# Optimization experiments

Measured on AMD Instinct MI355X. Metric: run time of the kernel, lower is better.

## Reference

```python
import jax, jax.numpy as jnp
import numpy as np

N_EMBD = 768
FULL_SIZE = 16 * N_EMBD   # 12288
K = 4 * N_EMBD            # iter_size = 3072 (top-k)
B, T = 8, 1024


def setup_inputs() -> dict:
    key = jax.random.key(0)
    k0, k1, k2, k3, k4 = jax.random.split(key, 5)
    s = lambda fan_in: 1.0 / np.sqrt(fan_in)
    return {
        "x": jax.random.normal(k0, (B, T, N_EMBD), dtype=jnp.float32),
        "w1": jax.random.normal(k1, (N_EMBD // 16, N_EMBD), dtype=jnp.float32) * s(N_EMBD),
        "w2": jax.random.normal(k2, (FULL_SIZE, N_EMBD // 16), dtype=jnp.float32) * s(N_EMBD // 16),
        "w_mfc": jax.random.normal(k3, (FULL_SIZE, N_EMBD), dtype=jnp.float32) * s(N_EMBD),
        "w_proj": jax.random.normal(k4, (N_EMBD, FULL_SIZE), dtype=jnp.float32) * s(FULL_SIZE),
    }


def _topk_mask(ck, k):
    # softmax -> top-k indices -> hard 0/1 mask (scatter of constant 1.0)
    probs = jax.nn.softmax(ck, axis=-1)
    _, idx = jax.lax.top_k(probs, k)            # (B, k)
    b = jnp.arange(probs.shape[0])[:, None]
    return jnp.zeros_like(probs).at[b, idx].set(1.0)


def reference(x, w1, w2, w_mfc, w_proj):
    # control net on sequence-mean pooled features
    pooled = x.mean(axis=1)                                  # (B, D)
    ck = jax.nn.relu(pooled @ w1.T) @ w2.T                   # (B, F)
    mask = _topk_mask(ck, K)                                 # (B, F) hard 0/1
    # DynamicMaskedLinear: bmm(x, (W*mask)^T) == (x @ W^T) * mask (0/1 output mask)
    h = jnp.einsum('btd,fd->btf', x, w_mfc) * mask[:, None, :]
    h = jax.nn.relu(h)
    out = jnp.einsum('btf,ef->bte', h, w_proj)               # (B, T, D)
    return out
```

## Files before the change

kernel.cpp:

```cpp
#include <hip/hip_runtime.h>

#define N_EMBD 768
#define FULL   12288
#define KSEL   3072
#define BATCH  8
#define TLEN   1024
#define HID    48

typedef short bf16x8 __attribute__((ext_vector_type(8)));
typedef float f32x4 __attribute__((ext_vector_type(4)));
typedef unsigned short u16x4 __attribute__((ext_vector_type(4)));
typedef unsigned short u16x8 __attribute__((ext_vector_type(8)));

#define MFMA(a, b, c) __builtin_amdgcn_mfma_f32_16x16x32_bf16((a), (b), (c), 0, 0, 0)
#define GLDS(g, l) __builtin_amdgcn_global_load_lds( \
    (const __attribute__((address_space(1))) void*)(const void*)(g), \
    (__attribute__((address_space(3))) void*)(void*)(l), 16, 0, 0)

__device__ __forceinline__ unsigned short f2bf(float f) {
  unsigned u = __float_as_uint(f);
  u += 0x7fffu + ((u >> 16) & 1u);
  return (unsigned short)(u >> 16);
}
__device__ __forceinline__ float bf2f(unsigned short h) {
  return __uint_as_float(((unsigned)h) << 16);
}

__global__ void split_pool_x(const float* __restrict__ x, unsigned short* __restrict__ xh,
                             float* __restrict__ partial) {
  const int s = blockIdx.x;
  const int b = blockIdx.y;
  const int d = blockIdx.z * 256 + threadIdx.x * 4;
  const float* base = x + ((size_t)(b * TLEN + s * 64)) * N_EMBD + d;
  float4 sum = {0.f, 0.f, 0.f, 0.f};
  for (int t = 0; t < 64; ++t) {
    const float4 v = *(const float4*)(base + (size_t)t * N_EMBD);
    sum.x += v.x; sum.y += v.y; sum.z += v.z; sum.w += v.w;
    u16x4 h;
    h.x = f2bf(v.x); h.y = f2bf(v.y); h.z = f2bf(v.z); h.w = f2bf(v.w);
    *(u16x4*)(xh + ((size_t)(b * TLEN + s * 64 + t)) * N_EMBD + d) = h;
  }
  float* pp = partial + (b * 16 + s) * N_EMBD + d;
  pp[0] = sum.x; pp[1] = sum.y; pp[2] = sum.z; pp[3] = sum.w;
}

__global__ __launch_bounds__(256) void control1_kernel(
    const float* __restrict__ partial, const float* __restrict__ w1, float* __restrict__ hid) {
  __shared__ float w1s[HID][385];
  __shared__ float ps[N_EMBD];
  const int b = blockIdx.x;
  const int tid = threadIdx.x;
  for (int d = tid; d < N_EMBD; d += 256) {
    float sum = 0.f;
    #pragma unroll
    for (int s = 0; s < 16; ++s) sum += partial[(b * 16 + s) * N_EMBD + d];
    ps[d] = sum * (1.f / TLEN);
  }
  float acc = 0.f;
  #pragma unroll
  for (int half = 0; half < 2; ++half) {
    __syncthreads();
    for (int i = tid; i < HID * 384; i += 256) {
      const int r = i / 384, c = i % 384;
      w1s[r][c] = w1[r * N_EMBD + half * 384 + c];
    }
    __syncthreads();
    if (tid < HID) {
      const float* pr = ps + half * 384;
      #pragma unroll 8
      for (int d2 = 0; d2 < 384; ++d2) acc = fmaf(pr[d2], w1s[tid][d2], acc);
    }
  }
  if (tid < HID) hid[b * HID + tid] = fmaxf(acc, 0.f);
}

__global__ void control2_kernel(const float* __restrict__ hid, const float* __restrict__ w2,
                                float* __restrict__ ck) {
  const int b = blockIdx.y;
  const int f = blockIdx.x * 256 + threadIdx.x;
  __shared__ float hid_s[HID];
  if (threadIdx.x < HID) hid_s[threadIdx.x] = hid[b * HID + threadIdx.x];
  __syncthreads();
  const float* wr = w2 + (size_t)f * HID;
  float acc = 0.f;
  #pragma unroll
  for (int j = 0; j < HID; ++j) acc = fmaf(hid_s[j], wr[j], acc);
  ck[b * FULL + f] = acc;
}

__global__ void topk_kernel(const float* __restrict__ ck, int* __restrict__ sel) {
  const int b = blockIdx.x;
  const int tid = threadIdx.x;
  const int lane = tid & 63, wv = tid >> 6;
  unsigned key[48];
  const int f_lo = tid * 48;
  #pragma unroll
  for (int i = 0; i < 48; ++i) {
    unsigned u = __float_as_uint(ck[b * FULL + f_lo + i]);
    key[i] = (u & 0x80000000u) ? ~u : (u | 0x80000000u);
  }
  __shared__ unsigned redw[4];
  __shared__ int sg[257], se[257];
  unsigned prefix = 0;
  int remaining = KSEL;
  for (int bit = 31; bit >= 0; --bit) {
    const unsigned want = prefix | (1u << bit);
    const unsigned shifted = want >> bit;
    int cnt = 0;
    #pragma unroll
    for (int i = 0; i < 48; ++i) cnt += ((key[i] >> bit) == shifted) ? 1 : 0;
    #pragma unroll
    for (int off = 1; off < 64; off <<= 1) cnt += __shfl_xor(cnt, off, 64);
    if (lane == 0) redw[wv] = (unsigned)cnt;
    __syncthreads();
    const int c = (int)(redw[0] + redw[1] + redw[2] + redw[3]);
    __syncthreads();
    if (c >= remaining) prefix = want;
    else remaining -= c;
  }
  const unsigned kth = prefix;
  int cg = 0, ce = 0;
  #pragma unroll
  for (int i = 0; i < 48; ++i) { cg += (key[i] > kth) ? 1 : 0; ce += (key[i] == kth) ? 1 : 0; }
  sg[tid] = cg; se[tid] = ce;
  __syncthreads();
  if (tid == 0) {
    int ag = 0, ae = 0;
    for (int i = 0; i < 256; ++i) {
      int tg = sg[i], te = se[i];
      sg[i] = ag; se[i] = ae;
      ag += tg; ae += te;
    }
    sg[256] = ag;
  }
  __syncthreads();
  const int ng = sg[256];
  int gpos = sg[tid], epos = se[tid];
  #pragma unroll
  for (int i = 0; i < 48; ++i) {
    const unsigned k = key[i];
    const int f = f_lo + i;
    if (k > kth) {
      sel[b * KSEL + (gpos++)] = f;
    } else if (k == kth) {
      const int p = ng + epos;
      if (p < KSEL) sel[b * KSEL + p] = f;
      ++epos;
    }
  }
}

__global__ void round_w_kernel(const float* __restrict__ src, unsigned short* __restrict__ dst, int n4) {
  const int idx = blockIdx.x * 256 + threadIdx.x;
  if (idx >= n4) return;
  const float4 v = ((const float4*)src)[idx];
  u16x4 h;
  h.x = f2bf(v.x); h.y = f2bf(v.y); h.z = f2bf(v.z); h.w = f2bf(v.w);
  ((u16x4*)dst)[idx] = h;
}

__global__ __launch_bounds__(256) void gather_wp_kernel(
    const float* __restrict__ wproj, const int* __restrict__ sel,
    unsigned short* __restrict__ wph) {
  __shared__ unsigned short row_s[FULL];
  const int e = blockIdx.x;
  const int tid = threadIdx.x;
  const float* wr = wproj + (size_t)e * FULL;
  #pragma unroll
  for (int i = 0; i < FULL / 4 / 256; ++i) {
    const int idx = tid + i * 256;
    const float4 v = ((const float4*)wr)[idx];
    u16x4 h;
    h.x = f2bf(v.x); h.y = f2bf(v.y); h.z = f2bf(v.z); h.w = f2bf(v.w);
    *(u16x4*)(row_s + idx * 4) = h;
  }
  __syncthreads();
  #pragma unroll
  for (int i = 0; i < 12; ++i) {
    const int idx = tid + i * 256;
    const int b = idx / 384, c = idx % 384;
    const int* sp = sel + b * KSEL + c * 8;
    const int4 s0 = ((const int4*)sp)[0];
    const int4 s1 = ((const int4*)sp)[1];
    u16x8 v;
    v[0] = row_s[s0.x]; v[1] = row_s[s0.y]; v[2] = row_s[s0.z]; v[3] = row_s[s0.w];
    v[4] = row_s[s1.x]; v[5] = row_s[s1.y]; v[6] = row_s[s1.z]; v[7] = row_s[s1.w];
    *(u16x8*)(wph + ((size_t)(b * N_EMBD + e)) * KSEL + c * 8) = v;
  }
}

__global__ __launch_bounds__(256) void gemm1_mfma(
    const unsigned short* __restrict__ xh, const unsigned short* __restrict__ wh,
    const int* __restrict__ sel, unsigned short* __restrict__ hh) {
  __shared__ __align__(16) char sm[32768];
  const int nx = TLEN / 128, ny = KSEL / 128;
  const int nwg = nx * ny * BATCH;
  int lin = blockIdx.x + nx * (blockIdx.y + ny * blockIdx.z);
  int swz = (lin & 7) * (nwg >> 3) + (lin >> 3);
  const int bx = swz % nx; int tmp = swz / nx;
  const int by = tmp % ny; const int b = tmp / ny;
  const int t0 = bx * 128, f0 = by * 128;

  const int tid = threadIdx.x;
  const int wv = tid >> 6, lane = tid & 63;
  const int srow = tid >> 2, sslot = tid & 3;
  const int wb = wv * 1024;

  const char* pxh = (const char*)xh;
  const char* pwh = (const char*)wh;
  const size_t aoff  = ((size_t)(b * TLEN + t0 + srow)) * 1536 + sslot * 16;
  const size_t aoff2 = aoff + (size_t)64 * 1536;
  const int* selb = sel + b * KSEL;
  const size_t boff  = (size_t)selb[f0 + srow] * 1536 + sslot * 16;
  const size_t boff2 = (size_t)selb[f0 + srow + 64] * 1536 + sslot * 16;

  const int fr = lane & 15, kg = lane >> 4;
  const int fo = fr * 64 + kg * 16;
  const int m0 = (wv >> 1) * 64, n0 = (wv & 1) * 64;

  f32x4 acc[4][4];
  const f32x4 z4 = {0.f, 0.f, 0.f, 0.f};
  #pragma unroll
  for (int mi = 0; mi < 4; ++mi)
    #pragma unroll
    for (int ni = 0; ni < 4; ++ni) acc[mi][ni] = z4;

  auto stage = [&](int bo, int d) {
    GLDS(pxh + aoff  + d, sm + bo + 0     + wb);
    GLDS(pxh + aoff2 + d, sm + bo + 4096  + wb);
    GLDS(pwh + boff  + d, sm + bo + 8192  + wb);
    GLDS(pwh + boff2 + d, sm + bo + 12288 + wb);
  };
  stage(0, 0);
  __syncthreads();
  const int NIT = N_EMBD * 2 / 64;
  for (int it = 0; it < NIT; ++it) {
    const int cur = (it & 1) ? 16384 : 0;
    if (it + 1 < NIT) stage(cur ^ 16384, (it + 1) * 64);
    bf16x8 ah[4], bh[4];
    #pragma unroll
    for (int i = 0; i < 4; ++i) {
      ah[i] = *(const bf16x8*)(sm + cur + 0    + (m0 + i * 16) * 64 + fo);
      bh[i] = *(const bf16x8*)(sm + cur + 8192 + (n0 + i * 16) * 64 + fo);
    }
    #pragma unroll
    for (int mi = 0; mi < 4; ++mi)
      #pragma unroll
      for (int ni = 0; ni < 4; ++ni)
        acc[mi][ni] = MFMA(ah[mi], bh[ni], acc[mi][ni]);
    __syncthreads();
  }
  unsigned short* lh = (unsigned short*)sm;
  const int rowg = lane >> 4, colc = lane & 15;
  #pragma unroll
  for (int mi = 0; mi < 4; ++mi)
    #pragma unroll
    for (int ni = 0; ni < 4; ++ni) {
      const int row = m0 + mi * 16 + rowg * 4;
      const int col = n0 + ni * 16 + colc;
      #pragma unroll
      for (int j = 0; j < 4; ++j)
        lh[(row + j) * 128 + col] = f2bf(fmaxf(acc[mi][ni][j], 0.f));
    }
  __syncthreads();
  const int orow = tid >> 4, oc = tid & 15;
  #pragma unroll
  for (int i2 = 0; i2 < 8; ++i2) {
    const int row = orow + i2 * 16;
    const u16x8 v = *(const u16x8*)&lh[row * 128 + oc * 8];
    *(u16x8*)(hh + ((size_t)(b * TLEN + t0 + row)) * KSEL + f0 + oc * 8) = v;
  }
}

__global__ __launch_bounds__(256) void gemm2_mfma(
    const unsigned short* __restrict__ hh, const unsigned short* __restrict__ wph,
    float* __restrict__ out) {
  __shared__ __align__(16) char sm[49152];
  const int lin = blockIdx.x;
  const int b = lin & 7;
  const int j = lin >> 3;
  const int bx = j & 7, by = j >> 3;
  const int t0 = bx * 128, e0 = by * 64;

  const int tid = threadIdx.x;
  const int wv = tid >> 6, lane = tid & 63;
  const int wb = wv * 1024;

  const char* pa = (const char*)hh;
  const char* pb = (const char*)wph;
  const size_t aoff  = ((size_t)(b * TLEN + t0 + (tid >> 2))) * 6144 + (tid & 3) * 16;
  const size_t aoff2 = aoff + (size_t)64 * 6144;
  const size_t boff  = ((size_t)(b * N_EMBD + e0 + (tid >> 2))) * 6144 + (tid & 3) * 16;

  const int fr = lane & 15, kg = lane >> 4;
  const int fo = fr * 64 + kg * 16;
  const int m0 = (wv >> 1) * 64, n0 = (wv & 1) * 32;

  f32x4 acc[4][2];
  const f32x4 z4 = {0.f, 0.f, 0.f, 0.f};
  #pragma unroll
  for (int mi = 0; mi < 4; ++mi)
    #pragma unroll
    for (int ni = 0; ni < 2; ++ni) acc[mi][ni] = z4;

  auto stage = [&](int bo, int d) {
    GLDS(pa + aoff  + d,      sm + bo + 0     + wb);
    GLDS(pa + aoff2 + d,      sm + bo + 4096  + wb);
    GLDS(pa + aoff  + d + 64, sm + bo + 8192  + wb);
    GLDS(pa + aoff2 + d + 64, sm + bo + 12288 + wb);
    GLDS(pb + boff  + d,      sm + bo + 16384 + wb);
    GLDS(pb + boff  + d + 64, sm + bo + 20480 + wb);
  };
  stage(0, 0);
  __syncthreads();
  const int NIT = KSEL * 2 / 128;
  for (int it = 0; it < NIT; ++it) {
    const int cur = (it & 1) ? 24576 : 0;
    if (it + 1 < NIT) stage(cur ^ 24576, (it + 1) * 128);
    bf16x8 ah[4][2], bh[2][2];
    #pragma unroll
    for (int i = 0; i < 4; ++i) {
      const int ra = (m0 + i * 16) * 64 + fo;
      ah[i][0] = *(const bf16x8*)(sm + cur + 0    + ra);
      ah[i][1] = *(const bf16x8*)(sm + cur + 8192 + ra);
    }
    #pragma unroll
    for (int i = 0; i < 2; ++i) {
      const int rb = (n0 + i * 16) * 64 + fo;
      bh[i][0] = *(const bf16x8*)(sm + cur + 16384 + rb);
      bh[i][1] = *(const bf16x8*)(sm + cur + 20480 + rb);
    }
    #pragma unroll
    for (int c = 0; c < 2; ++c)
      #pragma unroll
      for (int mi = 0; mi < 4; ++mi)
        #pragma unroll
        for (int ni = 0; ni < 2; ++ni)
          acc[mi][ni] = MFMA(ah[mi][c], bh[ni][c], acc[mi][ni]);
    __syncthreads();
  }
  const int rowg = lane >> 4, colc = lane & 15;
  #pragma unroll
  for (int mi = 0; mi < 4; ++mi)
    #pragma unroll
    for (int ni = 0; ni < 2; ++ni) {
      const int m = t0 + m0 + mi * 16 + rowg * 4;
      const int e = e0 + n0 + ni * 16 + colc;
      const size_t base = ((size_t)(b * TLEN + m)) * N_EMBD + e;
      #pragma unroll
      for (int jj = 0; jj < 4; ++jj)
        out[base + (size_t)jj * N_EMBD] = acc[mi][ni][jj];
    }
}

extern "C" void kernel_launch(void* const* d_in, const int* in_sizes, int n_in,
                              void* d_out, int out_size, void* d_ws, size_t ws_size,
                              hipStream_t stream) {
  const float* x      = (const float*)d_in[0];
  const float* w1     = (const float*)d_in[1];
  const float* w2     = (const float*)d_in[2];
  const float* w_mfc  = (const float*)d_in[3];
  const float* w_proj = (const float*)d_in[4];
  float* out = (float*)d_out;

  char* ws = (char*)d_ws;
  size_t off = 0;
  auto alloc = [&](size_t bytes) -> void* {
    void* p = ws + off;
    off += (bytes + 255) & ~(size_t)255;
    return p;
  };
  const size_t NX  = (size_t)BATCH * TLEN * N_EMBD;
  const size_t NW  = (size_t)FULL * N_EMBD;
  const size_t NWP = (size_t)BATCH * N_EMBD * KSEL;
  const size_t NH  = (size_t)BATCH * TLEN * KSEL;

  float* partial = (float*)alloc((size_t)BATCH * 16 * N_EMBD * 4);
  float* hid     = (float*)alloc((size_t)BATCH * HID * 4);
  float* ckbuf   = (float*)alloc((size_t)BATCH * FULL * 4);
  int*   sel     = (int*)  alloc((size_t)BATCH * KSEL * 4);
  unsigned short* xh  = (unsigned short*)alloc(NX * 2);
  unsigned short* wh  = (unsigned short*)alloc(NW * 2);
  unsigned short* wph = (unsigned short*)alloc(NWP * 2);
  unsigned short* hh  = (unsigned short*)alloc(NH * 2);

  split_pool_x<<<dim3(16, BATCH, 3), 64, 0, stream>>>(x, xh, partial);
  round_w_kernel<<<(int)(NW / 4 / 256), 256, 0, stream>>>(w_mfc, wh, (int)(NW / 4));
  control1_kernel<<<BATCH, 256, 0, stream>>>(partial, w1, hid);
  control2_kernel<<<dim3(FULL / 256, BATCH), 256, 0, stream>>>(hid, w2, ckbuf);
  topk_kernel<<<BATCH, 256, 0, stream>>>(ckbuf, sel);
  gather_wp_kernel<<<768, 256, 0, stream>>>(w_proj, sel, wph);
  gemm1_mfma<<<dim3(TLEN / 128, KSEL / 128, BATCH), 256, 0, stream>>>(xh, wh, sel, hh);
  gemm2_mfma<<<768, 256, 0, stream>>>(hh, wph, out);
}
```

Before: 324.1 us.

## Triple-buffer LDS staging in both GEMMs with explicit vmcnt waits and single barrier

Both MFMA GEMM kernels move from a double-buffered LDS pipeline with two __syncthreads per iteration to a three-stage ring. Loads are issued two iterations ahead, and each iteration waits with a partial s_waitcnt vmcnt before one s_barrier. The goal is to hide global-load latency better and cut barrier overhead. The cost is more shared memory per block (48KB and 72KB), which may lower occupancy, and the correctness now rests on hand-counted vmcnt values.

```diff
diff --git a/kernel.cpp b/kernel.cpp
--- a/kernel.cpp
+++ b/kernel.cpp
@@ -192,7 +192,7 @@
 __global__ __launch_bounds__(256) void gemm1_mfma(
     const unsigned short* __restrict__ xh, const unsigned short* __restrict__ wh,
     const int* __restrict__ sel, unsigned short* __restrict__ hh) {
-  __shared__ __align__(16) char sm[32768];
+  __shared__ __align__(16) char sm[49152];
   const int nx = TLEN / 128, ny = KSEL / 128;
   const int nwg = nx * ny * BATCH;
   int lin = blockIdx.x + nx * (blockIdx.y + ny * blockIdx.z);
@@ -225,18 +225,22 @@
     #pragma unroll
     for (int ni = 0; ni < 4; ++ni) acc[mi][ni] = z4;
 
-  auto stage = [&](int bo, int d) {
-    GLDS(pxh + aoff  + d, sm + bo + 0     + wb);
-    GLDS(pxh + aoff2 + d, sm + bo + 4096  + wb);
-    GLDS(pwh + boff  + d, sm + bo + 8192  + wb);
-    GLDS(pwh + boff2 + d, sm + bo + 12288 + wb);
+  auto stage = [&](int bo, int kb) {
+    GLDS(pxh + aoff  + kb, sm + bo + 0     + wb);
+    GLDS(pxh + aoff2 + kb, sm + bo + 4096  + wb);
+    GLDS(pwh + boff  + kb, sm + bo + 8192  + wb);
+    GLDS(pwh + boff2 + kb, sm + bo + 12288 + wb);
   };
+  const int NIT = N_EMBD * 2 / 64;
   stage(0, 0);
-  __syncthreads();
-  const int NIT = N_EMBD * 2 / 64;
+  stage(16384, 64);
   for (int it = 0; it < NIT; ++it) {
-    const int cur = (it & 1) ? 16384 : 0;
-    if (it + 1 < NIT) stage(cur ^ 16384, (it + 1) * 64);
+    if (it < NIT - 1) asm volatile("s_waitcnt vmcnt(4)" ::: "memory");
+    else              asm volatile("s_waitcnt vmcnt(0)" ::: "memory");
+    __builtin_amdgcn_s_barrier();
+    __builtin_amdgcn_sched_barrier(0);
+    const int cur = (it % 3) << 14;
+    if (it + 2 < NIT) stage(((it + 2) % 3) << 14, (it + 2) * 64);
     bf16x8 ah[4], bh[4];
     #pragma unroll
     for (int i = 0; i < 4; ++i) {
@@ -248,8 +252,8 @@
       #pragma unroll
       for (int ni = 0; ni < 4; ++ni)
         acc[mi][ni] = MFMA(ah[mi], bh[ni], acc[mi][ni]);
-    __syncthreads();
-  }
+  }
+  __syncthreads();
   unsigned short* lh = (unsigned short*)sm;
   const int rowg = lane >> 4, colc = lane & 15;
   #pragma unroll
@@ -275,7 +279,7 @@
 __global__ __launch_bounds__(256) void gemm2_mfma(
     const unsigned short* __restrict__ hh, const unsigned short* __restrict__ wph,
     float* __restrict__ out) {
-  __shared__ __align__(16) char sm[49152];
+  __shared__ __align__(16) char sm[73728];
   const int lin = blockIdx.x;
   const int b = lin & 7;
   const int j = lin >> 3;
@@ -311,12 +315,16 @@
     GLDS(pb + boff  + d,      sm + bo + 16384 + wb);
     GLDS(pb + boff  + d + 64, sm + bo + 20480 + wb);
   };
+  const int NIT = KSEL * 2 / 128;
   stage(0, 0);
-  __syncthreads();
-  const int NIT = KSEL * 2 / 128;
+  stage(24576, 128);
   for (int it = 0; it < NIT; ++it) {
-    const int cur = (it & 1) ? 24576 : 0;
-    if (it + 1 < NIT) stage(cur ^ 24576, (it + 1) * 128);
+    if (it < NIT - 1) asm volatile("s_waitcnt vmcnt(6)" ::: "memory");
+    else              asm volatile("s_waitcnt vmcnt(0)" ::: "memory");
+    __builtin_amdgcn_s_barrier();
+    __builtin_amdgcn_sched_barrier(0);
+    const int cur = (it % 3) * 24576;
+    if (it + 2 < NIT) stage(((it + 2) % 3) * 24576, (it + 2) * 128);
     bf16x8 ah[4][2], bh[2][2];
     #pragma unroll
     for (int i = 0; i < 4; ++i) {
@@ -337,7 +345,6 @@
         #pragma unroll
         for (int ni = 0; ni < 2; ++ni)
           acc[mi][ni] = MFMA(ah[mi][c], bh[ni][c], acc[mi][ni]);
-    __syncthreads();
   }
   const int rowg = lane >> 4, colc = lane & 15;
   #pragma unroll
```

After: 323.4 us. About the same (-0.2%).
